# Kernel tuning notes

Hardware: AMD Instinct MI355X
Metric: run time of the kernel (lower is better)

## Reference

```python
import jax, jax.numpy as jnp
import numpy as np

N_SLICES = 2  # init kwarg n_slices


def affine_grid_3d(theta, D, H, W):
    """torch.nn.functional.affine_grid for 5D output, align_corners=False.
    theta: [B,3,4]; returns grid [B,D,H,W,3] with last dim (x,y,z) ~ (W,H,D)."""
    xs = (jnp.arange(W, dtype=theta.dtype) + 0.5) * (2.0 / W) - 1.0
    ys = (jnp.arange(H, dtype=theta.dtype) + 0.5) * (2.0 / H) - 1.0
    zs = (jnp.arange(D, dtype=theta.dtype) + 0.5) * (2.0 / D) - 1.0
    zz, yy, xx = jnp.meshgrid(zs, ys, xs, indexing='ij')
    base = jnp.stack([xx, yy, zz, jnp.ones_like(xx)], axis=-1)  # [D,H,W,4]
    return jnp.einsum('bij,dhwj->bdhwi', theta, base)  # [B,D,H,W,3]


def grid_sample_3d_zeros(vol, grid):
    """torch.nn.functional.grid_sample, mode='bilinear' (trilinear for 5D),
    padding_mode='zeros', align_corners=False.
    vol: [B,C,D,H,W]; grid: [B,D,H,W,3] normalized xyz coords."""
    B, C, D, H, W = vol.shape
    ix = ((grid[..., 0] + 1.0) * W - 1.0) * 0.5
    iy = ((grid[..., 1] + 1.0) * H - 1.0) * 0.5
    iz = ((grid[..., 2] + 1.0) * D - 1.0) * 0.5
    ix0 = jnp.floor(ix); iy0 = jnp.floor(iy); iz0 = jnp.floor(iz)
    fx = ix - ix0; fy = iy - iy0; fz = iz - iz0

    def gather(v, z, y, x):  # v: [C,D,H,W], idx: [D,H,W] -> [C,D,H,W]
        return v[:, z, y, x]

    out = jnp.zeros((B, C, D, H, W), vol.dtype)
    for dz in (0, 1):
        for dy in (0, 1):
            for dx in (0, 1):
                xi = ix0 + dx; yi = iy0 + dy; zi = iz0 + dz
                w = (jnp.where(dx, fx, 1.0 - fx)
                     * jnp.where(dy, fy, 1.0 - fy)
                     * jnp.where(dz, fz, 1.0 - fz))
                valid = ((xi >= 0) & (xi < W) & (yi >= 0) & (yi < H)
                         & (zi >= 0) & (zi < D))
                xc = jnp.clip(xi, 0, W - 1).astype(jnp.int32)
                yc = jnp.clip(yi, 0, H - 1).astype(jnp.int32)
                zc = jnp.clip(zi, 0, D - 1).astype(jnp.int32)
                vals = jax.vmap(gather)(vol, zc, yc, xc)  # [B,C,D,H,W]
                out = out + vals * (w * valid)[:, None]
    return out


def skip_connector(x, b_grid_affines):
    B, C, SPAT, _ = x.shape
    # zero volume with the 2D slice stack placed at the central W-plane
    vol = jnp.zeros((B, C, SPAT, SPAT, SPAT), x.dtype).at[..., SPAT // 2].set(x)
    chunks = jnp.split(vol, N_SLICES, axis=1)
    outs = []
    for i in range(N_SLICES):
        aff = b_grid_affines[i].astype(jnp.float32)  # [B,4,4]
        # get_zooms: column norms of rotation block
        zooms = jnp.sqrt((aff[:, :3, :3] ** 2).sum(axis=1))  # [B,3]
        # rescale_rot_components_with_diag(aff, 1/zooms) == aff @ diag(1/zx,1/zy,1/zz,1)
        scale = jnp.concatenate([1.0 / zooms, jnp.ones((aff.shape[0], 1), aff.dtype)], axis=1)
        aff = aff * scale[:, None, :]
        theta = jnp.linalg.inv(aff)[:, :3, :]  # [B,3,4]
        grid = affine_grid_3d(theta, SPAT, SPAT, SPAT)
        outs.append(grid_sample_3d_zeros(chunks[i], grid))
    return jnp.concatenate(outs, axis=1)  # [B,C,SPAT,SPAT,SPAT]


def setup_inputs() -> dict:
    key = jax.random.key(0)
    k1, k2 = jax.random.split(key)
    B, C, SPAT = 2, 32, 96
    x = jax.random.normal(k1, (B, C, SPAT, SPAT), dtype=jnp.float32)
    # near-identity invertible homogeneous affines for the two views (SA, HLA)
    noise = 0.1 * jax.random.normal(k2, (2, B, 4, 4), dtype=jnp.float32)
    aff = jnp.eye(4, dtype=jnp.float32)[None, None] + noise
    aff = aff.at[..., 3, :].set(jnp.array([0.0, 0.0, 0.0, 1.0], dtype=jnp.float32))
    return {"x": x, "b_grid_affines": aff}


def reference(x, b_grid_affines):
    return skip_connector(x, b_grid_affines)
```

## Files before the change

### kernel.cpp

```cpp
#include <hip/hip_runtime.h>
#include <math.h>

#define SPAT 96
#define PLANE (SPAT*SPAT*SPAT)
#define IMG   (SPAT*SPAT)
#define OUT_FLOATS (64 * PLANE)

__device__ inline void invert4(const float m[16], float inv[16]) {
    inv[0]  =  m[5]*m[10]*m[15] - m[5]*m[11]*m[14] - m[9]*m[6]*m[15] + m[9]*m[7]*m[14] + m[13]*m[6]*m[11] - m[13]*m[7]*m[10];
    inv[4]  = -m[4]*m[10]*m[15] + m[4]*m[11]*m[14] + m[8]*m[6]*m[15] - m[8]*m[7]*m[14] - m[12]*m[6]*m[11] + m[12]*m[7]*m[10];
    inv[8]  =  m[4]*m[9]*m[15]  - m[4]*m[11]*m[13] - m[8]*m[5]*m[15] + m[8]*m[7]*m[13] + m[12]*m[5]*m[11] - m[12]*m[7]*m[9];
    inv[12] = -m[4]*m[9]*m[14]  + m[4]*m[10]*m[13] + m[8]*m[5]*m[14] - m[8]*m[6]*m[13] - m[12]*m[5]*m[10] + m[12]*m[6]*m[9];
    inv[1]  = -m[1]*m[10]*m[15] + m[1]*m[11]*m[14] + m[9]*m[2]*m[15] - m[9]*m[3]*m[14] - m[13]*m[2]*m[11] + m[13]*m[3]*m[10];
    inv[5]  =  m[0]*m[10]*m[15] - m[0]*m[11]*m[14] - m[8]*m[2]*m[15] + m[8]*m[3]*m[14] + m[12]*m[2]*m[11] - m[12]*m[3]*m[10];
    inv[9]  = -m[0]*m[9]*m[15]  + m[0]*m[11]*m[13] + m[8]*m[1]*m[15] - m[8]*m[3]*m[13] - m[12]*m[1]*m[11] + m[12]*m[3]*m[9];
    inv[13] =  m[0]*m[9]*m[14]  - m[0]*m[10]*m[13] - m[8]*m[1]*m[14] + m[8]*m[2]*m[13] + m[12]*m[1]*m[10] - m[12]*m[2]*m[9];
    inv[2]  =  m[1]*m[6]*m[15]  - m[1]*m[7]*m[14]  - m[5]*m[2]*m[15] + m[5]*m[3]*m[14] + m[13]*m[2]*m[7]  - m[13]*m[3]*m[6];
    inv[6]  = -m[0]*m[6]*m[15]  + m[0]*m[7]*m[14]  + m[4]*m[2]*m[15] - m[4]*m[3]*m[14] - m[12]*m[2]*m[7]  + m[12]*m[3]*m[6];
    inv[10] =  m[0]*m[5]*m[15]  - m[0]*m[7]*m[13]  - m[4]*m[1]*m[15] + m[4]*m[3]*m[13] + m[12]*m[1]*m[7]  - m[12]*m[3]*m[5];
    inv[14] = -m[0]*m[5]*m[14]  + m[0]*m[6]*m[13]  + m[4]*m[1]*m[14] - m[4]*m[2]*m[13] - m[12]*m[1]*m[6]  + m[12]*m[2]*m[5];
    inv[3]  = -m[1]*m[6]*m[11]  + m[1]*m[7]*m[10]  + m[5]*m[2]*m[11] - m[5]*m[3]*m[10] - m[9]*m[2]*m[7]   + m[9]*m[3]*m[6];
    inv[7]  =  m[0]*m[6]*m[11]  - m[0]*m[7]*m[10]  - m[4]*m[2]*m[11] + m[4]*m[3]*m[10] + m[8]*m[2]*m[7]   - m[8]*m[3]*m[6];
    inv[11] = -m[0]*m[5]*m[11]  + m[0]*m[7]*m[9]   + m[4]*m[1]*m[11] - m[4]*m[3]*m[9]  - m[8]*m[1]*m[7]   + m[8]*m[3]*m[5];
    inv[15] =  m[0]*m[5]*m[10]  - m[0]*m[6]*m[9]   - m[4]*m[1]*m[10] + m[4]*m[2]*m[9]  + m[8]*m[1]*m[6]   - m[8]*m[2]*m[5];
    float det  = m[0]*inv[0] + m[1]*inv[4] + m[2]*inv[8] + m[3]*inv[12];
    float rdet = 1.0f / det;
    for (int i = 0; i < 16; ++i) inv[i] *= rdet;
}

__global__ __launch_bounds__(256) void zero_kernel(float4* __restrict__ out) {
    const size_t n4 = OUT_FLOATS / 4;
    size_t i = (size_t)blockIdx.x * 256 + threadIdx.x;
    size_t stride = (size_t)gridDim.x * 256;
    float4 z = make_float4(0.f, 0.f, 0.f, 0.f);
    for (; i < n4; i += stride) out[i] = z;
}

__global__ __launch_bounds__(256) void slab_kernel(
        const float* __restrict__ xin,
        const float* __restrict__ aff_in,
        float* __restrict__ out) {
    __shared__ float Ms[12];
    int sb = blockIdx.y;
    if (threadIdx.x == 0) {
        float A[16];
        #pragma unroll
        for (int i = 0; i < 16; ++i) A[i] = aff_in[sb * 16 + i];
        #pragma unroll
        for (int j = 0; j < 3; ++j) {
            float z = sqrtf(A[0*4+j]*A[0*4+j] + A[1*4+j]*A[1*4+j] + A[2*4+j]*A[2*4+j]);
            float rz = 1.0f / z;
            #pragma unroll
            for (int i = 0; i < 4; ++i) A[i*4+j] *= rz;
        }
        float inv[16];
        invert4(A, inv);
        #pragma unroll
        for (int r = 0; r < 3; ++r) {
            float T0 = inv[r*4+0], T1 = inv[r*4+1], T2 = inv[r*4+2], T3 = inv[r*4+3];
            Ms[r*4+0] = T0;
            Ms[r*4+1] = T1;
            Ms[r*4+2] = T2;
            Ms[r*4+3] = -47.5f * (T0 + T1 + T2) + 48.0f * T3 + 47.5f;
        }
    }
    __syncthreads();

    int t    = blockIdx.x * 256 + threadIdx.x;
    int cg   = t & 3;
    int qpar = (t >> 2) & 1;
    int hd   = t >> 3;
    int h    = hd % SPAT;
    int d    = hd / SPAT;
    int s    = sb >> 1;
    int b    = sb & 1;

    float Mxw = Ms[0], Mxh = Ms[1], Mxd = Ms[2],  Mx0 = Ms[3];
    float Myw = Ms[4], Myh = Ms[5], Myd = Ms[6],  My0 = Ms[7];
    float Mzw = Ms[8], Mzh = Ms[9], Mzd = Ms[10], Mz0 = Ms[11];

    float fh = (float)h, fd = (float)d;
    float bx = Mxh * fh + Mxd * fd + Mx0;

    int wlo, whi;
    if (fabsf(Mxw) > 1e-6f) {
        float rMxw = 1.0f / Mxw;
        float w1 = (47.0f - bx) * rMxw;
        float w2 = (49.0f - bx) * rMxw;
        float wmin = fminf(w1, w2), wmax = fmaxf(w1, w2);
        wlo = max((int)ceilf(wmin), 0);
        whi = min((int)floorf(wmax), SPAT - 1);
    } else {
        bool in = fabsf(bx - 48.0f) < 1.0f;
        wlo = in ? 0 : 1;
        whi = in ? SPAT - 1 : 0;
    }
    if (wlo > whi) return;
    int qlo = (wlo >> 2) + qpar, qhi = whi >> 2;

    float by = Myh * fh + Myd * fd + My0;
    float bz = Mzh * fh + Mzd * fd + Mz0;

    size_t cbase = (size_t)(b * 32 + s * 16 + cg * 4);
    const float* img = xin + cbase * (size_t)IMG;
    float* op = out + cbase * (size_t)PLANE + ((size_t)d * SPAT + h) * SPAT;

    for (int q = qlo; q <= qhi; q += 2) {
        float v[4][4];
        #pragma unroll
        for (int j = 0; j < 4; ++j) {
            float fw = (float)(4 * q + j);
            float ix = Mxw * fw + bx;
            float wx = 1.0f - fabsf(ix - 48.0f);
            if (wx > 0.0f) {
                float iy = Myw * fw + by;
                float iz = Mzw * fw + bz;
                float yf = floorf(iy), zf = floorf(iz);
                float fy = iy - yf,    fz = iz - zf;
                int y0 = (int)yf, z0 = (int)zf;
                bool vy0 = (y0 >= 0)  & (y0 <  SPAT);
                bool vy1 = (y0 >= -1) & (y0 <  SPAT - 1);
                bool vz0 = (z0 >= 0)  & (z0 <  SPAT);
                bool vz1 = (z0 >= -1) & (z0 <  SPAT - 1);
                int y0c = min(max(y0, 0),     SPAT - 1);
                int y1c = min(max(y0 + 1, 0), SPAT - 1);
                int z0c = min(max(z0, 0),     SPAT - 1);
                int z1c = min(max(z0 + 1, 0), SPAT - 1);
                float wy0 = 1.0f - fy, wy1 = fy;
                float wz0 = 1.0f - fz, wz1 = fz;
                float w00 = wx * wz0 * wy0 * ((vz0 & vy0) ? 1.0f : 0.0f);
                float w01 = wx * wz0 * wy1 * ((vz0 & vy1) ? 1.0f : 0.0f);
                float w10 = wx * wz1 * wy0 * ((vz1 & vy0) ? 1.0f : 0.0f);
                float w11 = wx * wz1 * wy1 * ((vz1 & vy1) ? 1.0f : 0.0f);
                int o00 = z0c * SPAT + y0c, o01 = z0c * SPAT + y1c;
                int o10 = z1c * SPAT + y0c, o11 = z1c * SPAT + y1c;
                #pragma unroll
                for (int c = 0; c < 4; ++c) {
                    const float* ic = img + (size_t)c * IMG;
                    v[c][j] = w00 * ic[o00] + w01 * ic[o01]
                            + w10 * ic[o10] + w11 * ic[o11];
                }
            } else {
                #pragma unroll
                for (int c = 0; c < 4; ++c) v[c][j] = 0.0f;
            }
        }
        #pragma unroll
        for (int c = 0; c < 4; ++c) {
            *reinterpret_cast<float4*>(op + (size_t)c * PLANE + 4 * q) =
                make_float4(v[c][0], v[c][1], v[c][2], v[c][3]);
        }
    }
}

extern "C" void kernel_launch(void* const* d_in, const int* in_sizes, int n_in,
                              void* d_out, int out_size, void* d_ws, size_t ws_size,
                              hipStream_t stream) {
    const float* x   = (const float*)d_in[0];
    const float* aff = (const float*)d_in[1];
    float* out = (float*)d_out;

    zero_kernel<<<4096, 256, 0, stream>>>((float4*)out);

    dim3 grid(288, 4);
    slab_kernel<<<grid, 256, 0, stream>>>(x, aff, out);
}
```

Baseline: 237.2 us.

## Fuse zero-fill into slab kernel, skip zeroing slab-covered float4s, precompute inverses

```diff
diff --git a/kernel.cpp b/kernel.cpp
--- a/kernel.cpp
+++ b/kernel.cpp
@@ -4,7 +4,9 @@
 #define SPAT 96
 #define PLANE (SPAT*SPAT*SPAT)
 #define IMG   (SPAT*SPAT)
-#define OUT_FLOATS (64 * PLANE)
+#define SLAB_BLOCKS 1152
+#define ZERO_BLOCKS 4608
+#define K_ITERS 12
 
 __device__ inline void invert4(const float m[16], float inv[16]) {
     inv[0]  =  m[5]*m[10]*m[15] - m[5]*m[11]*m[14] - m[9]*m[6]*m[15] + m[9]*m[7]*m[14] + m[13]*m[6]*m[11] - m[13]*m[7]*m[10];
@@ -28,127 +30,169 @@
     for (int i = 0; i < 16; ++i) inv[i] *= rdet;
 }
 
-__global__ __launch_bounds__(256) void zero_kernel(float4* __restrict__ out) {
-    const size_t n4 = OUT_FLOATS / 4;
-    size_t i = (size_t)blockIdx.x * 256 + threadIdx.x;
-    size_t stride = (size_t)gridDim.x * 256;
-    float4 z = make_float4(0.f, 0.f, 0.f, 0.f);
-    for (; i < n4; i += stride) out[i] = z;
-}
-
-__global__ __launch_bounds__(256) void slab_kernel(
+__global__ void prep_kernel(const float* __restrict__ aff_in,
+                            float* __restrict__ ws) {
+    int t = threadIdx.x;
+    if (t >= 4) return;
+    float A[16];
+    #pragma unroll
+    for (int i = 0; i < 16; ++i) A[i] = aff_in[t * 16 + i];
+    #pragma unroll
+    for (int j = 0; j < 3; ++j) {
+        float z = sqrtf(A[0*4+j]*A[0*4+j] + A[1*4+j]*A[1*4+j] + A[2*4+j]*A[2*4+j]);
+        float rz = 1.0f / z;
+        #pragma unroll
+        for (int i = 0; i < 4; ++i) A[i*4+j] *= rz;
+    }
+    float inv[16];
+    invert4(A, inv);
+    float* M = ws + t * 16;
+    #pragma unroll
+    for (int r = 0; r < 3; ++r) {
+        float T0 = inv[r*4+0], T1 = inv[r*4+1], T2 = inv[r*4+2], T3 = inv[r*4+3];
+        M[r*4+0] = T0;
+        M[r*4+1] = T1;
+        M[r*4+2] = T2;
+        M[r*4+3] = -47.5f * (T0 + T1 + T2) + 48.0f * T3 + 47.5f;
+    }
+    float Mxw  = M[0];
+    float rMxw = 1.0f / Mxw;
+    float b47 = 47.0f * rMxw, b49 = 49.0f * rMxw;
+    M[12] = -rMxw;
+    M[13] = fminf(b47, b49) - 0.5f;
+    M[14] = fmaxf(b47, b49) + 0.5f;
+    M[15] = 0.0f;
+}
+
+__global__ __launch_bounds__(256) void fused_kernel(
         const float* __restrict__ xin,
-        const float* __restrict__ aff_in,
+        const float* __restrict__ ws,
         float* __restrict__ out) {
-    __shared__ float Ms[12];
-    int sb = blockIdx.y;
-    if (threadIdx.x == 0) {
-        float A[16];
-        #pragma unroll
-        for (int i = 0; i < 16; ++i) A[i] = aff_in[sb * 16 + i];
-        #pragma unroll
-        for (int j = 0; j < 3; ++j) {
-            float z = sqrtf(A[0*4+j]*A[0*4+j] + A[1*4+j]*A[1*4+j] + A[2*4+j]*A[2*4+j]);
-            float rz = 1.0f / z;
+    int bid = blockIdx.x;
+    if (bid < SLAB_BLOCKS) {
+        int sb  = bid / 288;
+        int rem = bid - sb * 288;
+        int t    = rem * 256 + threadIdx.x;
+        int cg   = t & 3;
+        int qpar = (t >> 2) & 1;
+        int hd   = t >> 3;
+        int h    = hd % SPAT;
+        int d    = hd / SPAT;
+        int s    = sb >> 1;
+        int b    = sb & 1;
+
+        const float* M = ws + sb * 16;
+        float Mxw = M[0], Mxh = M[1], Mxd = M[2],  Mx0 = M[3];
+        float Myw = M[4], Myh = M[5], Myd = M[6],  My0 = M[7];
+        float Mzw = M[8], Mzh = M[9], Mzd = M[10], Mz0 = M[11];
+
+        float fh = (float)h, fd = (float)d;
+        float bx = Mxh * fh + Mxd * fd + Mx0;
+
+        int wlo, whi;
+        if (fabsf(Mxw) > 1e-6f) {
+            float rMxw = 1.0f / Mxw;
+            float w1 = (47.0f - bx) * rMxw;
+            float w2 = (49.0f - bx) * rMxw;
+            float wmin = fminf(w1, w2), wmax = fmaxf(w1, w2);
+            wlo = max((int)ceilf(wmin), 0);
+            whi = min((int)floorf(wmax), SPAT - 1);
+        } else {
+            bool in = fabsf(bx - 48.0f) < 1.0f;
+            wlo = in ? 0 : 1;
+            whi = in ? SPAT - 1 : 0;
+        }
+        if (wlo > whi) return;
+        int qlo = (wlo >> 2) + qpar, qhi = whi >> 2;
+
+        float by = Myh * fh + Myd * fd + My0;
+        float bz = Mzh * fh + Mzd * fd + Mz0;
+
+        size_t cbase = (size_t)(b * 32 + s * 16 + cg * 4);
+        const float* img = xin + cbase * (size_t)IMG;
+        float* op = out + cbase * (size_t)PLANE + ((size_t)d * SPAT + h) * SPAT;
+
+        for (int q = qlo; q <= qhi; q += 2) {
+            float v[4][4];
             #pragma unroll
-            for (int i = 0; i < 4; ++i) A[i*4+j] *= rz;
-        }
-        float inv[16];
-        invert4(A, inv);
-        #pragma unroll
-        for (int r = 0; r < 3; ++r) {
-            float T0 = inv[r*4+0], T1 = inv[r*4+1], T2 = inv[r*4+2], T3 = inv[r*4+3];
-            Ms[r*4+0] = T0;
-            Ms[r*4+1] = T1;
-            Ms[r*4+2] = T2;
-            Ms[r*4+3] = -47.5f * (T0 + T1 + T2) + 48.0f * T3 + 47.5f;
-        }
-    }
-    __syncthreads();
-
-    int t    = blockIdx.x * 256 + threadIdx.x;
-    int cg   = t & 3;
-    int qpar = (t >> 2) & 1;
-    int hd   = t >> 3;
-    int h    = hd % SPAT;
-    int d    = hd / SPAT;
-    int s    = sb >> 1;
-    int b    = sb & 1;
-
-    float Mxw = Ms[0], Mxh = Ms[1], Mxd = Ms[2],  Mx0 = Ms[3];
-    float Myw = Ms[4], Myh = Ms[5], Myd = Ms[6],  My0 = Ms[7];
-    float Mzw = Ms[8], Mzh = Ms[9], Mzd = Ms[10], Mz0 = Ms[11];
-
-    float fh = (float)h, fd = (float)d;
-    float bx = Mxh * fh + Mxd * fd + Mx0;
-
-    int wlo, whi;
-    if (fabsf(Mxw) > 1e-6f) {
-        float rMxw = 1.0f / Mxw;
-        float w1 = (47.0f - bx) * rMxw;
-        float w2 = (49.0f - bx) * rMxw;
-        float wmin = fminf(w1, w2), wmax = fmaxf(w1, w2);
-        wlo = max((int)ceilf(wmin), 0);
-        whi = min((int)floorf(wmax), SPAT - 1);
-    } else {
-        bool in = fabsf(bx - 48.0f) < 1.0f;
-        wlo = in ? 0 : 1;
-        whi = in ? SPAT - 1 : 0;
-    }
-    if (wlo > whi) return;
-    int qlo = (wlo >> 2) + qpar, qhi = whi >> 2;
-
-    float by = Myh * fh + Myd * fd + My0;
-    float bz = Mzh * fh + Mzd * fd + Mz0;
-
-    size_t cbase = (size_t)(b * 32 + s * 16 + cg * 4);
-    const float* img = xin + cbase * (size_t)IMG;
-    float* op = out + cbase * (size_t)PLANE + ((size_t)d * SPAT + h) * SPAT;
-
-    for (int q = qlo; q <= qhi; q += 2) {
-        float v[4][4];
-        #pragma unroll
-        for (int j = 0; j < 4; ++j) {
-            float fw = (float)(4 * q + j);
-            float ix = Mxw * fw + bx;
-            float wx = 1.0f - fabsf(ix - 48.0f);
-            if (wx > 0.0f) {
-                float iy = Myw * fw + by;
-                float iz = Mzw * fw + bz;
-                float yf = floorf(iy), zf = floorf(iz);
-                float fy = iy - yf,    fz = iz - zf;
-                int y0 = (int)yf, z0 = (int)zf;
-                bool vy0 = (y0 >= 0)  & (y0 <  SPAT);
-                bool vy1 = (y0 >= -1) & (y0 <  SPAT - 1);
-                bool vz0 = (z0 >= 0)  & (z0 <  SPAT);
-                bool vz1 = (z0 >= -1) & (z0 <  SPAT - 1);
-                int y0c = min(max(y0, 0),     SPAT - 1);
-                int y1c = min(max(y0 + 1, 0), SPAT - 1);
-                int z0c = min(max(z0, 0),     SPAT - 1);
-                int z1c = min(max(z0 + 1, 0), SPAT - 1);
-                float wy0 = 1.0f - fy, wy1 = fy;
-                float wz0 = 1.0f - fz, wz1 = fz;
-                float w00 = wx * wz0 * wy0 * ((vz0 & vy0) ? 1.0f : 0.0f);
-                float w01 = wx * wz0 * wy1 * ((vz0 & vy1) ? 1.0f : 0.0f);
-                float w10 = wx * wz1 * wy0 * ((vz1 & vy0) ? 1.0f : 0.0f);
-                float w11 = wx * wz1 * wy1 * ((vz1 & vy1) ? 1.0f : 0.0f);
-                int o00 = z0c * SPAT + y0c, o01 = z0c * SPAT + y1c;
-                int o10 = z1c * SPAT + y0c, o11 = z1c * SPAT + y1c;
-                #pragma unroll
-                for (int c = 0; c < 4; ++c) {
-                    const float* ic = img + (size_t)c * IMG;
-                    v[c][j] = w00 * ic[o00] + w01 * ic[o01]
-                            + w10 * ic[o10] + w11 * ic[o11];
+            for (int j = 0; j < 4; ++j) {
+                float fw = (float)(4 * q + j);
+                float ix = Mxw * fw + bx;
+                float wx = 1.0f - fabsf(ix - 48.0f);
+                if (wx > 0.0f) {
+                    float iy = Myw * fw + by;
+                    float iz = Mzw * fw + bz;
+                    float yf = floorf(iy), zf = floorf(iz);
+                    float fy = iy - yf,    fz = iz - zf;
+                    int y0 = (int)yf, z0 = (int)zf;
+                    bool vy0 = (y0 >= 0)  & (y0 <  SPAT);
+                    bool vy1 = (y0 >= -1) & (y0 <  SPAT - 1);
+                    bool vz0 = (z0 >= 0)  & (z0 <  SPAT);
+                    bool vz1 = (z0 >= -1) & (z0 <  SPAT - 1);
+                    int y0c = min(max(y0, 0),     SPAT - 1);
+                    int y1c = min(max(y0 + 1, 0), SPAT - 1);
+                    int z0c = min(max(z0, 0),     SPAT - 1);
+                    int z1c = min(max(z0 + 1, 0), SPAT - 1);
+                    float wy0 = 1.0f - fy, wy1 = fy;
+                    float wz0 = 1.0f - fz, wz1 = fz;
+                    float w00 = wx * wz0 * wy0 * ((vz0 & vy0) ? 1.0f : 0.0f);
+                    float w01 = wx * wz0 * wy1 * ((vz0 & vy1) ? 1.0f : 0.0f);
+                    float w10 = wx * wz1 * wy0 * ((vz1 & vy0) ? 1.0f : 0.0f);
+                    float w11 = wx * wz1 * wy1 * ((vz1 & vy1) ? 1.0f : 0.0f);
+                    int o00 = z0c * SPAT + y0c, o01 = z0c * SPAT + y1c;
+                    int o10 = z1c * SPAT + y0c, o11 = z1c * SPAT + y1c;
+                    #pragma unroll
+                    for (int c = 0; c < 4; ++c) {
+                        const float* ic = img + (size_t)c * IMG;
+                        v[c][j] = w00 * ic[o00] + w01 * ic[o01]
+                                + w10 * ic[o10] + w11 * ic[o11];
+                    }
+                } else {
+                    #pragma unroll
+                    for (int c = 0; c < 4; ++c) v[c][j] = 0.0f;
                 }
-            } else {
-                #pragma unroll
-                for (int c = 0; c < 4; ++c) v[c][j] = 0.0f;
+            }
+            #pragma unroll
+            for (int c = 0; c < 4; ++c) {
+                *reinterpret_cast<float4*>(op + (size_t)c * PLANE + 4 * q) =
+                    make_float4(v[c][0], v[c][1], v[c][2], v[c][3]);
             }
         }
+    } else {
+        int zid   = bid - SLAB_BLOCKS;
+        int sbz   = zid / 1152;
+        int inner = zid - sbz * 1152;
+        int q0    = (inner / 9) * 12;
+        int gslot = inner % 9;
+        int g     = gslot * 256 + threadIdx.x;
+        int h     = g / 24;
+        int w4    = g - 24 * h;
+        int s     = sbz >> 1, b = sbz & 1;
+
+        const float* M = ws + sbz * 16;
+        float Mxh = M[1], Mxd = M[2], Mx0 = M[3];
+        float a = M[12], bmin = M[13], bmax = M[14];
+
+        float fh = (float)h;
+        float f0 = (float)(4 * w4);
+        float f3 = f0 + 3.0f;
+
+        int CB = (b * 32 + s * 16) * SPAT;
+        float* ptr = out + (size_t)(CB + q0) * IMG + 4 * g;
+
+        float4 z4 = make_float4(0.f, 0.f, 0.f, 0.f);
+        int q = q0;
         #pragma unroll
-        for (int c = 0; c < 4; ++c) {
-            *reinterpret_cast<float4*>(op + (size_t)c * PLANE + 4 * q) =
-                make_float4(v[c][0], v[c][1], v[c][2], v[c][3]);
+        for (int k = 0; k < K_ITERS; ++k, ++q) {
+            int d = q % SPAT;
+            float fd = (float)d;
+            float u  = Mxd * fd + Mx0;
+            float bx = Mxh * fh + u;
+            float m_ = a * bx;
+            float wmin = m_ + bmin, wmax = m_ + bmax;
+            if (!((f3 >= wmin) & (f0 <= wmax)))
+                *reinterpret_cast<float4*>(ptr) = z4;
+            ptr += IMG;
         }
     }
 }
@@ -159,9 +203,8 @@
     const float* x   = (const float*)d_in[0];
     const float* aff = (const float*)d_in[1];
     float* out = (float*)d_out;
-
-    zero_kernel<<<4096, 256, 0, stream>>>((float4*)out);
-
-    dim3 grid(288, 4);
-    slab_kernel<<<grid, 256, 0, stream>>>(x, aff, out);
-}
+    float* M   = (float*)d_ws;
+
+    prep_kernel<<<1, 64, 0, stream>>>(aff, M);
+    fused_kernel<<<SLAB_BLOCKS + ZERO_BLOCKS, 256, 0, stream>>>(x, M, out);
+}
```

New measurement: 262.1 us. +10.5%, slower.
